# Performance work log

Measured on AMD Instinct MI355X. Metric: run time of the kernel, lower is better.

The kernel has to match this reference:

```python
import jax, jax.numpy as jnp
import numpy as np

B, M, T, D, V = 16, 4096, 4, 256, 40000
HOPS, NLAYER, CONV_MAX = 3, 3, 512
PAD = 1  # PAD_token: embedding row zeroed (padding_idx)


def setup_inputs() -> dict:
    key = jax.random.key(0)
    ks = jax.random.split(key, 10)
    story = jax.random.randint(ks[0], (B, M, T), 0, V)
    conv_len = jax.random.randint(ks[1], (B,), 1, CONV_MAX)
    kb_len = jax.random.randint(ks[2], (B,), 0, M - CONV_MAX)
    query = jax.random.normal(ks[3], (B, 1, D), jnp.float32)
    history_outputs = jax.random.normal(ks[4], (B, CONV_MAX, D), jnp.float32)
    query_vector = jax.random.normal(ks[5], (B, D), jnp.float32)
    global_pointer = jax.random.uniform(ks[6], (B, M), jnp.float32)
    # hop+1 embedding tables, N(0, 0.1), padding row zeroed
    C_emb = jax.random.normal(ks[7], (HOPS + 1, V, D), jnp.float32) * 0.1
    C_emb = C_emb.at[:, PAD, :].set(0.0)
    Tg_w = jax.random.normal(ks[8], (HOPS + 1, D, D), jnp.float32) * 0.05
    Tg_b = jnp.zeros((HOPS + 1, D), jnp.float32)
    FW_w = jax.random.normal(ks[9], (D, D), jnp.float32) * 0.05
    FW_b = jnp.zeros((D,), jnp.float32)
    return dict(story=story, kb_len=kb_len, conv_len=conv_len, query=query,
                history_outputs=history_outputs, query_vector=query_vector,
                global_pointer=global_pointer, C_emb=C_emb, Tg_w=Tg_w,
                Tg_b=Tg_b, FW_w=FW_w, FW_b=FW_b)


def _add_lm(mem, kb_len, conv_len, hist):
    # mem: [B,M,D]; add hist[b, 0:conv_len[b]] into mem[b, kb_len[b]:kb_len[b]+conv_len[b]]
    j = jnp.arange(mem.shape[1])[None, :]                       # [1,M]
    start = kb_len[:, None]
    mask = (j >= start) & (j < start + conv_len[:, None])       # [B,M]
    idx = jnp.clip(j - start, 0, hist.shape[1] - 1)             # [B,M]
    gathered = jnp.take_along_axis(hist, idx[..., None], axis=1)  # [B,M,D]
    return mem + jnp.where(mask[..., None], gathered, 0.0)


def _embed(table, story, kb_len, conv_len, hist):
    # bag-of-words over the mem-token axis, then LM-embedding add
    e = jnp.sum(table[story], axis=2)                           # [B,M,D]
    return _add_lm(e, kb_len, conv_len, hist)


def reference(story, kb_len, conv_len, query, history_outputs, query_vector,
              global_pointer, C_emb, Tg_w, Tg_b, FW_w, FW_b):
    # ---- load_memory (eval mode: dropout is identity; ablationH/G = False) ----
    q = query[:, 0, :]                                          # [B,D]
    last_u = None
    m_story = None
    for layer in range(NLAYER):
        iq = q
        if layer > 0:
            g = jax.nn.sigmoid(iq @ Tg_w[0].T + Tg_b[0])
            iq = last_u[0] * g + iq * (1.0 - g)
        u = [iq]
        m_story = []
        embC = None
        for hop in range(HOPS):
            embA = _embed(C_emb[hop], story, kb_len, conv_len, history_outputs)
            logit = jnp.einsum('bmd,bd->bm', embA, u[-1])
            prob = jax.nn.softmax(logit, axis=1)
            embC = _embed(C_emb[hop + 1], story, kb_len, conv_len, history_outputs)
            o_k = jnp.einsum('bm,bmd->bd', prob, embC)
            u_k = u[-1] + o_k
            if layer > 0:
                g = jax.nn.sigmoid(u_k @ Tg_w[hop + 1].T + Tg_b[hop + 1])
                u_k = last_u[hop + 1] * g + u_k * (1.0 - g)
            u.append(u_k)
            m_story.append(embA)
        m_story.append(embC)
        last_u = u
        q = jax.nn.relu(u[-1] @ FW_w.T + FW_b)
    # ---- forward (decoder-side read over last layer's memories) ----
    uf = query_vector
    psoft = None
    logits = None
    for hop in range(HOPS):
        mA = m_story[hop] * global_pointer[:, :, None]
        logits = jnp.einsum('bmd,bd->bm', mA, uf)
        psoft = jax.nn.softmax(logits, axis=1)
        mC = m_story[hop + 1] * global_pointer[:, :, None]
        uf = uf + jnp.einsum('bm,bmd->bd', psoft, mC)
    return (psoft, logits, uf, m_story[-1])
```

## Files before the change

kernel.cpp:

```cpp
#include <hip/hip_runtime.h>
#include <math.h>

#define Bdim 16
#define Mdim 4096
#define Tdim 4
#define Ddim 256
#define Vdim 40000
#define CONVMAX 512

#define DOT_VT 64
#define DOT_TILES (Vdim / DOT_VT)
#define DOT_KC 64
#define HD_JPB 32
#define HD_TILES (Bdim * (CONVMAX / HD_JPB))
#define LG_TILES (Bdim * Mdim / 256)
#define ZW_BLOCKS (Vdim * Bdim / 1024)
#define PW_BLOCKS (Bdim * CONVMAX / 1024)
#define WS_VT 50
#define WS_TILES (Vdim / WS_VT)
#define WH_JPB 64
#define WH_TILES (Bdim * (CONVMAX / WH_JPB))
#define UF_CH 8
#define UF_PER (WS_TILES / UF_CH)
#define MT 32
#define ATT_CH (Mdim / MT)
#define ATT_TILES (Bdim * ATT_CH)

typedef float f32x4 __attribute__((ext_vector_type(4)));
static __device__ inline void nt_store4(float* p, float4 v) {
    f32x4 x = {v.x, v.y, v.z, v.w};
    __builtin_nontemporal_store(x, (f32x4*)p);
}
static __device__ inline void nt_store1(float* p, float v) {
    __builtin_nontemporal_store(v, p);
}

static __device__ inline void combine_stats(const float* __restrict__ blockmax,
                                            const float* __restrict__ blocksum,
                                            int b, float* M_out, float* rs_out) {
    float M = -INFINITY;
#pragma unroll
    for (int jj = 0; jj < 16; ++jj) M = fmaxf(M, blockmax[b * 16 + jj]);
    float S = 0.f;
#pragma unroll
    for (int jj = 0; jj < 16; ++jj) S += blocksum[b * 16 + jj] * expf(blockmax[b * 16 + jj] - M);
    *M_out = M;
    *rs_out = 1.0f / S;
}

__global__ void init_kernel(const float* __restrict__ qv, float* __restrict__ uf) {
    int b = blockIdx.x, i = threadIdx.x;
    uf[(size_t)b * Ddim + i] = qv[(size_t)b * Ddim + i];
}

__global__ void dot_kernel(const float* __restrict__ tab, const float* __restrict__ uf,
                           const float* __restrict__ hist,
                           float* __restrict__ D, float* __restrict__ Hdot) {
    int bid = blockIdx.x, tid = threadIdx.x;
    if (bid < DOT_TILES) {
        __shared__ __align__(16) float tl[DOT_VT][DOT_KC + 4];
        __shared__ __align__(16) float ufl[Bdim][DOT_KC + 4];
        int v0 = bid * DOT_VT;
        int vA = (tid >> 3) * 2, vB = vA + 1;
        int bA = (tid & 7) * 2,  bB = bA + 1;
        float aA0 = 0.f, aA1 = 0.f, aB0 = 0.f, aB1 = 0.f;
        for (int kc = 0; kc < Ddim; kc += DOT_KC) {
            __syncthreads();
#pragma unroll
            for (int i = 0; i < 4; ++i) {
                int idx = tid + i * 256;
                int r = idx >> 4, c4 = idx & 15;
                *(float4*)(&tl[r][c4 * 4]) =
                    *(const float4*)(tab + (size_t)(v0 + r) * Ddim + kc + c4 * 4);
            }
            {
                int r = tid >> 4, c4 = tid & 15;
                *(float4*)(&ufl[r][c4 * 4]) =
                    *(const float4*)(uf + (size_t)r * Ddim + kc + c4 * 4);
            }
            __syncthreads();
#pragma unroll
            for (int k4 = 0; k4 < DOT_KC / 4; ++k4) {
                const float4 a  = *(const float4*)(&tl[vA][k4 * 4]);
                const float4 c  = *(const float4*)(&tl[vB][k4 * 4]);
                const float4 u0 = *(const float4*)(&ufl[bA][k4 * 4]);
                const float4 u1 = *(const float4*)(&ufl[bB][k4 * 4]);
                aA0 += a.x*u0.x + a.y*u0.y + a.z*u0.z + a.w*u0.w;
                aA1 += a.x*u1.x + a.y*u1.y + a.z*u1.z + a.w*u1.w;
                aB0 += c.x*u0.x + c.y*u0.y + c.z*u0.z + c.w*u0.w;
                aB1 += c.x*u1.x + c.y*u1.y + c.z*u1.z + c.w*u1.w;
            }
        }
        size_t base = (size_t)(v0 + vA) * Bdim;
        D[base + bA] = aA0;  D[base + bB] = aA1;
        D[base + Bdim + bA] = aB0;  D[base + Bdim + bB] = aB1;
    } else {
        int r = bid - DOT_TILES;
        int b = r >> 4, j0 = (r & 15) * HD_JPB;
        int wave = tid >> 6, lane = tid & 63;
        const float4 u = *(const float4*)(uf + (size_t)b * Ddim + lane * 4);
        for (int j = j0 + wave; j < j0 + HD_JPB; j += 4) {
            const float4 h = *(const float4*)(hist + ((size_t)b * CONVMAX + j) * Ddim + lane * 4);
            float s = h.x*u.x + h.y*u.y + h.z*u.z + h.w*u.w;
#pragma unroll
            for (int off = 32; off > 0; off >>= 1) s += __shfl_xor(s, off, 64);
            if (lane == 0) Hdot[b * CONVMAX + j] = s;
        }
    }
}

__global__ void logit_stats_kernel(const int* __restrict__ story, const int* __restrict__ kb_len,
                                   const int* __restrict__ conv_len, const float* __restrict__ D,
                                   const float* __restrict__ Hdot, const float* __restrict__ gp,
                                   float* __restrict__ lgbuf, float* __restrict__ blockmax,
                                   float* __restrict__ blocksum, float* __restrict__ w,
                                   float* __restrict__ pwin) {
    int bid = blockIdx.x, tid = threadIdx.x;
    if (bid >= LG_TILES) {
        int r = bid - LG_TILES;
        if (r < ZW_BLOCKS) {
            *(float4*)(w + (size_t)r * 1024 + tid * 4) = make_float4(0.f, 0.f, 0.f, 0.f);
        } else {
            *(float4*)(pwin + (size_t)(r - ZW_BLOCKS) * 1024 + tid * 4) = make_float4(0.f, 0.f, 0.f, 0.f);
        }
        return;
    }
    int row = bid * 256 + tid;
    int b = row >> 12, m = row & (Mdim - 1);
    const int4 st = *(const int4*)(story + (size_t)row * Tdim);
    float l = D[st.x*Bdim + b] + D[st.y*Bdim + b] + D[st.z*Bdim + b] + D[st.w*Bdim + b];
    unsigned j = (unsigned)(m - kb_len[b]);
    if (j < (unsigned)conv_len[b]) l += Hdot[b * CONVMAX + j];
    l *= gp[row];
    lgbuf[row] = l;
    __shared__ float sh[256];
    sh[tid] = l; __syncthreads();
    for (int s = 128; s > 0; s >>= 1) { if (tid < s) sh[tid] = fmaxf(sh[tid], sh[tid + s]); __syncthreads(); }
    float bm = sh[0]; __syncthreads();
    sh[tid] = expf(l - bm); __syncthreads();
    for (int s = 128; s > 0; s >>= 1) { if (tid < s) sh[tid] += sh[tid + s]; __syncthreads(); }
    if (tid == 0) { blockmax[bid] = bm; blocksum[bid] = sh[0]; }
}

__global__ void scatter_kernel(const int* __restrict__ story, const int* __restrict__ kb_len,
                               const int* __restrict__ conv_len, const float* __restrict__ logits,
                               const float* __restrict__ blockmax, const float* __restrict__ blocksum,
                               const float* __restrict__ gp, float* __restrict__ w,
                               float* __restrict__ pwin) {
    int bid = blockIdx.x, tid = threadIdx.x;
    int b = bid >> 4;
    float M, rs;
    combine_stats(blockmax, blocksum, b, &M, &rs);
    int row = bid * 256 + tid;
    int m = row & (Mdim - 1);
    float p = expf(logits[row] - M) * rs * gp[row];
    const int4 st = *(const int4*)(story + (size_t)row * Tdim);
    atomicAdd(&w[st.x * Bdim + b], p);
    atomicAdd(&w[st.y * Bdim + b], p);
    atomicAdd(&w[st.z * Bdim + b], p);
    atomicAdd(&w[st.w * Bdim + b], p);
    unsigned j = (unsigned)(m - kb_len[b]);
    if (j < (unsigned)conv_len[b]) pwin[b * CONVMAX + j] = p;
}

__global__ void wsum_kernel(const float* __restrict__ tab, const float* __restrict__ w,
                            const float* __restrict__ pwin, const float* __restrict__ hist,
                            float* __restrict__ partial, float* __restrict__ histpart) {
    int bid = blockIdx.x, tid = threadIdx.x;
    if (bid < WS_TILES) {
        __shared__ float wsl[WS_VT * Bdim];
        int v0 = bid * WS_VT;
        for (int i = tid; i < WS_VT * Bdim; i += 256) wsl[i] = w[(size_t)v0 * Bdim + i];
        __syncthreads();
        int wave = tid >> 6, lane = tid & 63;
        int b0 = wave * 4, d4 = lane * 4;
        float4 a0 = make_float4(0.f,0.f,0.f,0.f), a1 = a0, a2 = a0, a3 = a0;
        for (int v = 0; v < WS_VT; ++v) {
            const float4 t = *(const float4*)(tab + (size_t)(v0 + v) * Ddim + d4);
            float w0 = wsl[v*Bdim + b0],   w1 = wsl[v*Bdim + b0+1];
            float w2 = wsl[v*Bdim + b0+2], w3 = wsl[v*Bdim + b0+3];
            a0.x += w0*t.x; a0.y += w0*t.y; a0.z += w0*t.z; a0.w += w0*t.w;
            a1.x += w1*t.x; a1.y += w1*t.y; a1.z += w1*t.z; a1.w += w1*t.w;
            a2.x += w2*t.x; a2.y += w2*t.y; a2.z += w2*t.z; a2.w += w2*t.w;
            a3.x += w3*t.x; a3.y += w3*t.y; a3.z += w3*t.z; a3.w += w3*t.w;
        }
        *(float4*)(&partial[((size_t)(b0+0) * WS_TILES + bid) * Ddim + d4]) = a0;
        *(float4*)(&partial[((size_t)(b0+1) * WS_TILES + bid) * Ddim + d4]) = a1;
        *(float4*)(&partial[((size_t)(b0+2) * WS_TILES + bid) * Ddim + d4]) = a2;
        *(float4*)(&partial[((size_t)(b0+3) * WS_TILES + bid) * Ddim + d4]) = a3;
    } else {
        int r = bid - WS_TILES;
        int b = r >> 3, c = r & 7, j0 = c * WH_JPB;
        __shared__ float sp[WH_JPB];
        if (tid < WH_JPB) sp[tid] = pwin[b * CONVMAX + j0 + tid];
        __syncthreads();
        float acc = 0.f;
        const float* hb = hist + ((size_t)b * CONVMAX + j0) * Ddim + tid;
#pragma unroll 8
        for (int j = 0; j < WH_JPB; ++j) acc += sp[j] * hb[(size_t)j * Ddim];
        histpart[((size_t)b * UF_CH + c) * Ddim + tid] = acc;
    }
}

__global__ void ufred_kernel(const float* __restrict__ partial, const float* __restrict__ histpart,
                             float* __restrict__ uf) {
    int b = blockIdx.x >> 3, c = blockIdx.x & 7;
    int tid = threadIdx.x;
    float acc = 0.f;
    const float* base = partial + ((size_t)b * WS_TILES + c * UF_PER) * Ddim + tid;
#pragma unroll 4
    for (int i = 0; i < UF_PER; ++i) acc += base[(size_t)i * Ddim];
    acc += histpart[((size_t)b * UF_CH + c) * Ddim + tid];
    atomicAdd(&uf[(size_t)b * Ddim + tid], acc);
}

__global__ void att_kernel(const int* __restrict__ story, const int* __restrict__ kb_len,
                           const int* __restrict__ conv_len, const float* __restrict__ hist,
                           const float* __restrict__ tab, const float* __restrict__ logits,
                           const float* __restrict__ blockmax, const float* __restrict__ blocksum,
                           const float* __restrict__ gp,
                           float* __restrict__ attpart, float* __restrict__ out_m,
                           float* __restrict__ out_psoft) {
    int bid = blockIdx.x;
    int b  = bid >> 7;
    int m0 = (bid & (ATT_CH - 1)) * MT;
    int tid = threadIdx.x, wave = tid >> 6, lane = tid & 63;
    int d4 = lane * 4;
    __shared__ float prob[MT];
    __shared__ float4 red[4][64];
    if (tid < MT) {
        float M, rs;
        combine_stats(blockmax, blocksum, b, &M, &rs);
        size_t row = (size_t)b * Mdim + m0 + tid;
        float pn = expf(logits[row] - M) * rs;
        nt_store1(out_psoft + row, pn);
        prob[tid] = pn * gp[row];
    }
    __syncthreads();
    int kb = kb_len[b], cl = conv_len[b];
    float4 acc = make_float4(0.f, 0.f, 0.f, 0.f);
#pragma unroll 2
    for (int mm = wave; mm < MT; mm += 4) {
        int m = m0 + mm;
        size_t row = (size_t)b * Mdim + m;
        const int* st = story + row * Tdim;
        float4 v = make_float4(0.f, 0.f, 0.f, 0.f);
#pragma unroll
        for (int t = 0; t < Tdim; ++t) {
            const float4 wv = *(const float4*)(tab + (size_t)st[t] * Ddim + d4);
            v.x += wv.x; v.y += wv.y; v.z += wv.z; v.w += wv.w;
        }
        if (m >= kb && m < kb + cl) {
            const float4 h = *(const float4*)(hist + ((size_t)b * CONVMAX + (m - kb)) * Ddim + d4);
            v.x += h.x; v.y += h.y; v.z += h.z; v.w += h.w;
        }
        nt_store4(out_m + row * Ddim + d4, v);
        float p = prob[mm];
        acc.x += p * v.x; acc.y += p * v.y; acc.z += p * v.z; acc.w += p * v.w;
    }
    red[wave][lane] = acc;
    __syncthreads();
    if (wave == 0) {
        float4 a0 = red[0][lane], a1 = red[1][lane], a2 = red[2][lane], a3 = red[3][lane];
        float4 t4;
        t4.x = a0.x + a1.x + a2.x + a3.x;
        t4.y = a0.y + a1.y + a2.y + a3.y;
        t4.z = a0.z + a1.z + a2.z + a3.z;
        t4.w = a0.w + a1.w + a2.w + a3.w;
        *(float4*)(&attpart[((size_t)b * ATT_CH + (bid & (ATT_CH - 1))) * Ddim + d4]) = t4;
    }
}

__global__ void attred_kernel(const float* __restrict__ attpart, float* __restrict__ uf) {
    int b = blockIdx.x >> 2, c = blockIdx.x & 3;
    int tid = threadIdx.x;
    float acc = 0.f;
    const float* base = attpart + ((size_t)b * ATT_CH + c * 32) * Ddim + tid;
#pragma unroll 4
    for (int i = 0; i < 32; ++i) acc += base[(size_t)i * Ddim];
    atomicAdd(&uf[(size_t)b * Ddim + tid], acc);
}

extern "C" void kernel_launch(void* const* d_in, const int* in_sizes, int n_in,
                              void* d_out, int out_size, void* d_ws, size_t ws_size,
                              hipStream_t stream) {
    const int*   story        = (const int*)d_in[0];
    const int*   kb_len       = (const int*)d_in[1];
    const int*   conv_len     = (const int*)d_in[2];
    const float* hist         = (const float*)d_in[4];
    const float* query_vector = (const float*)d_in[5];
    const float* gp           = (const float*)d_in[6];
    const float* C_emb        = (const float*)d_in[7];

    float* out        = (float*)d_out;
    float* out_psoft  = out;
    float* out_logits = out + (size_t)Bdim * Mdim;
    float* out_uf     = out + 2 * (size_t)Bdim * Mdim;
    float* out_m      = out + 2 * (size_t)Bdim * Mdim + (size_t)Bdim * Ddim;

    float* wsp = (float*)d_ws;
    float* D        = wsp;
    float* w        = D + (size_t)Vdim * Bdim;
    float* Hdot     = w + (size_t)Vdim * Bdim;
    float* pwin     = Hdot + (size_t)Bdim * CONVMAX;
    float* logits   = pwin + (size_t)Bdim * CONVMAX;
    float* blockmax = logits + (size_t)Bdim * Mdim;
    float* blocksum = blockmax + 256;
    float* partial  = blocksum + 256;
    float* histpart = partial + (size_t)Bdim * WS_TILES * Ddim;
    float* attpart  = histpart + (size_t)Bdim * UF_CH * Ddim;

    const size_t TAB = (size_t)Vdim * Ddim;
    const float* tab[4] = { C_emb, C_emb + TAB, C_emb + 2*TAB, C_emb + 3*TAB };

    init_kernel<<<Bdim, Ddim, 0, stream>>>(query_vector, out_uf);

    for (int h = 0; h < 2; ++h) {
        const float* ufsrc = (h == 0) ? query_vector : out_uf;
        dot_kernel<<<DOT_TILES + HD_TILES, 256, 0, stream>>>(tab[h], ufsrc, hist, D, Hdot);
        logit_stats_kernel<<<LG_TILES + ZW_BLOCKS + PW_BLOCKS, 256, 0, stream>>>(
            story, kb_len, conv_len, D, Hdot, gp, logits, blockmax, blocksum, w, pwin);
        scatter_kernel<<<LG_TILES, 256, 0, stream>>>(story, kb_len, conv_len, logits,
                                                     blockmax, blocksum, gp, w, pwin);
        wsum_kernel<<<WS_TILES + WH_TILES, 256, 0, stream>>>(tab[h + 1], w, pwin, hist,
                                                             partial, histpart);
        ufred_kernel<<<Bdim * UF_CH, 256, 0, stream>>>(partial, histpart, out_uf);
    }

    dot_kernel<<<DOT_TILES + HD_TILES, 256, 0, stream>>>(tab[2], out_uf, hist, D, Hdot);
    logit_stats_kernel<<<LG_TILES, 256, 0, stream>>>(
        story, kb_len, conv_len, D, Hdot, gp, out_logits, blockmax, blocksum, nullptr, nullptr);
    att_kernel<<<ATT_TILES, 256, 0, stream>>>(story, kb_len, conv_len, hist, tab[3],
                                              out_logits, blockmax, blocksum, gp,
                                              attpart, out_m, out_psoft);
    attred_kernel<<<Bdim * 4, 256, 0, stream>>>(attpart, out_uf);
}
```

Baseline: 419.4 us.

## Spread final-hop memory embedding tiles across earlier kernels as filler blocks

The embedding of the last table (out_m, the [B,M,D] gather-sum plus history add) does not depend on the hop state, so it is split into 1024 tiles and computed as extra blocks appended to the earlier dot, stats, scatter, wsum and ufred launches. The final attention kernel then only reads out_m back and does the weighted sum, and the init copy is merged into the first dot launch. The aim is to fill idle or underused CUs in the small, latency-bound launches and shorten the critical path at the end. The cost is an extra 64 MB read of out_m in the final kernel (no longer written nontemporally) and more contention inside the earlier kernels.

New measurement: 482.5 us. +15.1%, slower.

```diff
diff --git a/kernel.cpp b/kernel.cpp
--- a/kernel.cpp
+++ b/kernel.cpp
@@ -22,15 +22,12 @@
 #define WH_TILES (Bdim * (CONVMAX / WH_JPB))
 #define UF_CH 8
 #define UF_PER (WS_TILES / UF_CH)
-#define MT 32
-#define ATT_CH (Mdim / MT)
-#define ATT_TILES (Bdim * ATT_CH)
+#define E3_MT 64
+#define E3_TILES (Bdim * Mdim / E3_MT)
+#define AL_MT 64
+#define AL_TILES (Bdim * Mdim / AL_MT)
 
 typedef float f32x4 __attribute__((ext_vector_type(4)));
-static __device__ inline void nt_store4(float* p, float4 v) {
-    f32x4 x = {v.x, v.y, v.z, v.w};
-    __builtin_nontemporal_store(x, (f32x4*)p);
-}
 static __device__ inline void nt_store1(float* p, float v) {
     __builtin_nontemporal_store(v, p);
 }
@@ -48,14 +45,39 @@
     *rs_out = 1.0f / S;
 }
 
-__global__ void init_kernel(const float* __restrict__ qv, float* __restrict__ uf) {
-    int b = blockIdx.x, i = threadIdx.x;
-    uf[(size_t)b * Ddim + i] = qv[(size_t)b * Ddim + i];
+static __device__ void e3_tile_body(int tile, const int* __restrict__ story,
+                                    const int* __restrict__ kb_len, const int* __restrict__ conv_len,
+                                    const float* __restrict__ hist, const float* __restrict__ tab3,
+                                    float* __restrict__ out_m, int tid) {
+    int b = tile >> 6;
+    int m0 = (tile & 63) * E3_MT;
+    int wave = tid >> 6, lane = tid & 63, d4 = lane * 4;
+    int kb = kb_len[b], cl = conv_len[b];
+    for (int mm = wave; mm < E3_MT; mm += 4) {
+        int m = m0 + mm;
+        size_t row = (size_t)b * Mdim + m;
+        const int* st = story + row * Tdim;
+        float4 v = make_float4(0.f, 0.f, 0.f, 0.f);
+#pragma unroll
+        for (int t = 0; t < Tdim; ++t) {
+            const float4 wv = *(const float4*)(tab3 + (size_t)st[t] * Ddim + d4);
+            v.x += wv.x; v.y += wv.y; v.z += wv.z; v.w += wv.w;
+        }
+        if (m >= kb && m < kb + cl) {
+            const float4 h = *(const float4*)(hist + ((size_t)b * CONVMAX + (m - kb)) * Ddim + d4);
+            v.x += h.x; v.y += h.y; v.z += h.z; v.w += h.w;
+        }
+        *(float4*)(out_m + row * Ddim + d4) = v;
+    }
 }
 
 __global__ void dot_kernel(const float* __restrict__ tab, const float* __restrict__ uf,
                            const float* __restrict__ hist,
-                           float* __restrict__ D, float* __restrict__ Hdot) {
+                           float* __restrict__ D, float* __restrict__ Hdot,
+                           const float* __restrict__ qv, float* __restrict__ uf_out,
+                           const int* __restrict__ story, const int* __restrict__ kb_len,
+                           const int* __restrict__ conv_len, const float* __restrict__ tab3,
+                           float* __restrict__ out_m, int init_blocks, int e3_base, int e3_count) {
     int bid = blockIdx.x, tid = threadIdx.x;
     if (bid < DOT_TILES) {
         __shared__ __align__(16) float tl[DOT_VT][DOT_KC + 4];
@@ -94,7 +116,7 @@
         size_t base = (size_t)(v0 + vA) * Bdim;
         D[base + bA] = aA0;  D[base + bB] = aA1;
         D[base + Bdim + bA] = aB0;  D[base + Bdim + bB] = aB1;
-    } else {
+    } else if (bid < DOT_TILES + HD_TILES) {
         int r = bid - DOT_TILES;
         int b = r >> 4, j0 = (r & 15) * HD_JPB;
         int wave = tid >> 6, lane = tid & 63;
@@ -106,6 +128,13 @@
             for (int off = 32; off > 0; off >>= 1) s += __shfl_xor(s, off, 64);
             if (lane == 0) Hdot[b * CONVMAX + j] = s;
         }
+    } else if (bid < DOT_TILES + HD_TILES + init_blocks) {
+        int b = bid - (DOT_TILES + HD_TILES);
+        uf_out[(size_t)b * Ddim + tid] = qv[(size_t)b * Ddim + tid];
+    } else {
+        int r = bid - (DOT_TILES + HD_TILES + init_blocks);
+        if (r < e3_count)
+            e3_tile_body(e3_base + r, story, kb_len, conv_len, hist, tab3, out_m, tid);
     }
 }
 
@@ -114,14 +143,20 @@
                                    const float* __restrict__ Hdot, const float* __restrict__ gp,
                                    float* __restrict__ lgbuf, float* __restrict__ blockmax,
                                    float* __restrict__ blocksum, float* __restrict__ w,
-                                   float* __restrict__ pwin) {
+                                   float* __restrict__ pwin, const float* __restrict__ hist,
+                                   const float* __restrict__ tab3, float* __restrict__ out_m,
+                                   int e3_base, int e3_count) {
     int bid = blockIdx.x, tid = threadIdx.x;
     if (bid >= LG_TILES) {
         int r = bid - LG_TILES;
-        if (r < ZW_BLOCKS) {
-            *(float4*)(w + (size_t)r * 1024 + tid * 4) = make_float4(0.f, 0.f, 0.f, 0.f);
-        } else {
-            *(float4*)(pwin + (size_t)(r - ZW_BLOCKS) * 1024 + tid * 4) = make_float4(0.f, 0.f, 0.f, 0.f);
+        int zb = w ? (ZW_BLOCKS + PW_BLOCKS) : 0;
+        if (r < zb) {
+            if (r < ZW_BLOCKS)
+                *(float4*)(w + (size_t)r * 1024 + tid * 4) = make_float4(0.f, 0.f, 0.f, 0.f);
+            else
+                *(float4*)(pwin + (size_t)(r - ZW_BLOCKS) * 1024 + tid * 4) = make_float4(0.f, 0.f, 0.f, 0.f);
+        } else if (r - zb < e3_count) {
+            e3_tile_body(e3_base + (r - zb), story, kb_len, conv_len, hist, tab3, out_m, tid);
         }
         return;
     }
@@ -146,8 +181,16 @@
                                const int* __restrict__ conv_len, const float* __restrict__ logits,
                                const float* __restrict__ blockmax, const float* __restrict__ blocksum,
                                const float* __restrict__ gp, float* __restrict__ w,
-                               float* __restrict__ pwin) {
-    int bid = blockIdx.x, tid = threadIdx.x;
+                               float* __restrict__ pwin, const float* __restrict__ hist,
+                               const float* __restrict__ tab3, float* __restrict__ out_m,
+                               int e3_base, int e3_count) {
+    int bid = blockIdx.x, tid = threadIdx.x;
+    if (bid >= LG_TILES) {
+        int r = bid - LG_TILES;
+        if (r < e3_count)
+            e3_tile_body(e3_base + r, story, kb_len, conv_len, hist, tab3, out_m, tid);
+        return;
+    }
     int b = bid >> 4;
     float M, rs;
     combine_stats(blockmax, blocksum, b, &M, &rs);
@@ -165,7 +208,10 @@
 
 __global__ void wsum_kernel(const float* __restrict__ tab, const float* __restrict__ w,
                             const float* __restrict__ pwin, const float* __restrict__ hist,
-                            float* __restrict__ partial, float* __restrict__ histpart) {
+                            float* __restrict__ partial, float* __restrict__ histpart,
+                            const int* __restrict__ story, const int* __restrict__ kb_len,
+                            const int* __restrict__ conv_len, const float* __restrict__ tab3,
+                            float* __restrict__ out_m, int e3_base, int e3_count) {
     int bid = blockIdx.x, tid = threadIdx.x;
     if (bid < WS_TILES) {
         __shared__ float wsl[WS_VT * Bdim];
@@ -188,7 +234,7 @@
         *(float4*)(&partial[((size_t)(b0+1) * WS_TILES + bid) * Ddim + d4]) = a1;
         *(float4*)(&partial[((size_t)(b0+2) * WS_TILES + bid) * Ddim + d4]) = a2;
         *(float4*)(&partial[((size_t)(b0+3) * WS_TILES + bid) * Ddim + d4]) = a3;
-    } else {
+    } else if (bid < WS_TILES + WH_TILES) {
         int r = bid - WS_TILES;
         int b = r >> 3, c = r & 7, j0 = c * WH_JPB;
         __shared__ float sp[WH_JPB];
@@ -199,13 +245,26 @@
 #pragma unroll 8
         for (int j = 0; j < WH_JPB; ++j) acc += sp[j] * hb[(size_t)j * Ddim];
         histpart[((size_t)b * UF_CH + c) * Ddim + tid] = acc;
+    } else {
+        int r = bid - (WS_TILES + WH_TILES);
+        if (r < e3_count)
+            e3_tile_body(e3_base + r, story, kb_len, conv_len, hist, tab3, out_m, tid);
     }
 }
 
 __global__ void ufred_kernel(const float* __restrict__ partial, const float* __restrict__ histpart,
-                             float* __restrict__ uf) {
-    int b = blockIdx.x >> 3, c = blockIdx.x & 7;
-    int tid = threadIdx.x;
+                             float* __restrict__ uf, const int* __restrict__ story,
+                             const int* __restrict__ kb_len, const int* __restrict__ conv_len,
+                             const float* __restrict__ hist, const float* __restrict__ tab3,
+                             float* __restrict__ out_m, int e3_base, int e3_count) {
+    int bid = blockIdx.x, tid = threadIdx.x;
+    if (bid >= Bdim * UF_CH) {
+        int r = bid - Bdim * UF_CH;
+        if (r < e3_count)
+            e3_tile_body(e3_base + r, story, kb_len, conv_len, hist, tab3, out_m, tid);
+        return;
+    }
+    int b = bid >> 3, c = bid & 7;
     float acc = 0.f;
     const float* base = partial + ((size_t)b * WS_TILES + c * UF_PER) * Ddim + tid;
 #pragma unroll 4
@@ -214,21 +273,18 @@
     atomicAdd(&uf[(size_t)b * Ddim + tid], acc);
 }
 
-__global__ void att_kernel(const int* __restrict__ story, const int* __restrict__ kb_len,
-                           const int* __restrict__ conv_len, const float* __restrict__ hist,
-                           const float* __restrict__ tab, const float* __restrict__ logits,
-                           const float* __restrict__ blockmax, const float* __restrict__ blocksum,
-                           const float* __restrict__ gp,
-                           float* __restrict__ attpart, float* __restrict__ out_m,
-                           float* __restrict__ out_psoft) {
+__global__ void att_lite_kernel(const float* __restrict__ out_m, const float* __restrict__ logits,
+                                const float* __restrict__ blockmax, const float* __restrict__ blocksum,
+                                const float* __restrict__ gp,
+                                float* __restrict__ attpart, float* __restrict__ out_psoft) {
     int bid = blockIdx.x;
-    int b  = bid >> 7;
-    int m0 = (bid & (ATT_CH - 1)) * MT;
+    int b  = bid >> 6;
+    int m0 = (bid & 63) * AL_MT;
     int tid = threadIdx.x, wave = tid >> 6, lane = tid & 63;
     int d4 = lane * 4;
-    __shared__ float prob[MT];
+    __shared__ float prob[AL_MT];
     __shared__ float4 red[4][64];
-    if (tid < MT) {
+    if (tid < AL_MT) {
         float M, rs;
         combine_stats(blockmax, blocksum, b, &M, &rs);
         size_t row = (size_t)b * Mdim + m0 + tid;
@@ -237,24 +293,11 @@
         prob[tid] = pn * gp[row];
     }
     __syncthreads();
-    int kb = kb_len[b], cl = conv_len[b];
     float4 acc = make_float4(0.f, 0.f, 0.f, 0.f);
-#pragma unroll 2
-    for (int mm = wave; mm < MT; mm += 4) {
-        int m = m0 + mm;
-        size_t row = (size_t)b * Mdim + m;
-        const int* st = story + row * Tdim;
-        float4 v = make_float4(0.f, 0.f, 0.f, 0.f);
-#pragma unroll
-        for (int t = 0; t < Tdim; ++t) {
-            const float4 wv = *(const float4*)(tab + (size_t)st[t] * Ddim + d4);
-            v.x += wv.x; v.y += wv.y; v.z += wv.z; v.w += wv.w;
-        }
-        if (m >= kb && m < kb + cl) {
-            const float4 h = *(const float4*)(hist + ((size_t)b * CONVMAX + (m - kb)) * Ddim + d4);
-            v.x += h.x; v.y += h.y; v.z += h.z; v.w += h.w;
-        }
-        nt_store4(out_m + row * Ddim + d4, v);
+#pragma unroll 4
+    for (int mm = wave; mm < AL_MT; mm += 4) {
+        size_t row = (size_t)b * Mdim + m0 + mm;
+        const float4 v = *(const float4*)(out_m + row * Ddim + d4);
         float p = prob[mm];
         acc.x += p * v.x; acc.y += p * v.y; acc.z += p * v.z; acc.w += p * v.w;
     }
@@ -267,17 +310,17 @@
         t4.y = a0.y + a1.y + a2.y + a3.y;
         t4.z = a0.z + a1.z + a2.z + a3.z;
         t4.w = a0.w + a1.w + a2.w + a3.w;
-        *(float4*)(&attpart[((size_t)b * ATT_CH + (bid & (ATT_CH - 1))) * Ddim + d4]) = t4;
+        *(float4*)(&attpart[(size_t)bid * Ddim + d4]) = t4;
     }
 }
 
 __global__ void attred_kernel(const float* __restrict__ attpart, float* __restrict__ uf) {
-    int b = blockIdx.x >> 2, c = blockIdx.x & 3;
+    int b = blockIdx.x >> 2, q = blockIdx.x & 3;
     int tid = threadIdx.x;
     float acc = 0.f;
-    const float* base = attpart + ((size_t)b * ATT_CH + c * 32) * Ddim + tid;
+    const float* base = attpart + ((size_t)(b * 64 + q * 16)) * Ddim + tid;
 #pragma unroll 4
-    for (int i = 0; i < 32; ++i) acc += base[(size_t)i * Ddim];
+    for (int i = 0; i < 16; ++i) acc += base[(size_t)i * Ddim];
     atomicAdd(&uf[(size_t)b * Ddim + tid], acc);
 }
 
@@ -313,25 +356,43 @@
     const size_t TAB = (size_t)Vdim * Ddim;
     const float* tab[4] = { C_emb, C_emb + TAB, C_emb + 2*TAB, C_emb + 3*TAB };
 
-    init_kernel<<<Bdim, Ddim, 0, stream>>>(query_vector, out_uf);
+    const int e3b[9] = {0, 256, 384, 512, 704, 768, 896, 960, 992};
+    const int e3c[9] = {256, 128, 128, 192, 64, 128, 64, 32, 32};
 
     for (int h = 0; h < 2; ++h) {
         const float* ufsrc = (h == 0) ? query_vector : out_uf;
-        dot_kernel<<<DOT_TILES + HD_TILES, 256, 0, stream>>>(tab[h], ufsrc, hist, D, Hdot);
-        logit_stats_kernel<<<LG_TILES + ZW_BLOCKS + PW_BLOCKS, 256, 0, stream>>>(
-            story, kb_len, conv_len, D, Hdot, gp, logits, blockmax, blocksum, w, pwin);
-        scatter_kernel<<<LG_TILES, 256, 0, stream>>>(story, kb_len, conv_len, logits,
-                                                     blockmax, blocksum, gp, w, pwin);
-        wsum_kernel<<<WS_TILES + WH_TILES, 256, 0, stream>>>(tab[h + 1], w, pwin, hist,
-                                                             partial, histpart);
-        ufred_kernel<<<Bdim * UF_CH, 256, 0, stream>>>(partial, histpart, out_uf);
-    }
-
-    dot_kernel<<<DOT_TILES + HD_TILES, 256, 0, stream>>>(tab[2], out_uf, hist, D, Hdot);
+        int k = h * 5;
+        int initb = (h == 0) ? Bdim : 0;
+        dot_kernel<<<DOT_TILES + HD_TILES + initb + e3c[k], 256, 0, stream>>>(
+            tab[h], ufsrc, hist, D, Hdot, query_vector, out_uf,
+            story, kb_len, conv_len, tab[3], out_m, initb, e3b[k], e3c[k]);
+        logit_stats_kernel<<<LG_TILES + ZW_BLOCKS + PW_BLOCKS + e3c[k+1], 256, 0, stream>>>(
+            story, kb_len, conv_len, D, Hdot, gp, logits, blockmax, blocksum, w, pwin,
+            hist, tab[3], out_m, e3b[k+1], e3c[k+1]);
+        scatter_kernel<<<LG_TILES + e3c[k+2], 256, 0, stream>>>(
+            story, kb_len, conv_len, logits, blockmax, blocksum, gp, w, pwin,
+            hist, tab[3], out_m, e3b[k+2], e3c[k+2]);
+        wsum_kernel<<<WS_TILES + WH_TILES + e3c[k+3], 256, 0, stream>>>(
+            tab[h + 1], w, pwin, hist, partial, histpart,
+            story, kb_len, conv_len, tab[3], out_m, e3b[k+3], e3c[k+3]);
+        if (h == 0) {
+            ufred_kernel<<<Bdim * UF_CH + e3c[k+4], 256, 0, stream>>>(
+                partial, histpart, out_uf, story, kb_len, conv_len, hist,
+                tab[3], out_m, e3b[k+4], e3c[k+4]);
+        } else {
+            ufred_kernel<<<Bdim * UF_CH, 256, 0, stream>>>(
+                partial, histpart, out_uf, story, kb_len, conv_len, hist,
+                tab[3], out_m, 0, 0);
+        }
+    }
+
+    dot_kernel<<<DOT_TILES + HD_TILES, 256, 0, stream>>>(
+        tab[2], out_uf, hist, D, Hdot, query_vector, out_uf,
+        story, kb_len, conv_len, tab[3], out_m, 0, 0, 0);
     logit_stats_kernel<<<LG_TILES, 256, 0, stream>>>(
-        story, kb_len, conv_len, D, Hdot, gp, out_logits, blockmax, blocksum, nullptr, nullptr);
-    att_kernel<<<ATT_TILES, 256, 0, stream>>>(story, kb_len, conv_len, hist, tab[3],
-                                              out_logits, blockmax, blocksum, gp,
-                                              attpart, out_m, out_psoft);
+        story, kb_len, conv_len, D, Hdot, gp, out_logits, blockmax, blocksum,
+        nullptr, nullptr, hist, tab[3], out_m, 0, 0);
+    att_lite_kernel<<<AL_TILES, 256, 0, stream>>>(
+        out_m, out_logits, blockmax, blocksum, gp, attpart, out_psoft);
     attred_kernel<<<Bdim * 4, 256, 0, stream>>>(attpart, out_uf);
 }
```
